# Kernel tuning notes

Measured on AMD Instinct MI355X. Metric: run time of the kernel, lower is better.

The kernel has to match this reference:

```python
import jax, jax.numpy as jnp
import numpy as np

N = 50000          # num nodes
E = 800000         # num edges
NUM_CLASSES = 40
FEAT_DIM = 256
FEAT_HID = 64
DEG_HID = 32
HID = 128
IN_CH = NUM_CLASSES + FEAT_HID + DEG_HID  # 136
MAX_DEG = 256      # degree-embedding table size (clip; random graph max deg << 256)


def _init_linear(key, fan_in, fan_out):
    kw, kb = jax.random.split(key)
    s = 1.0 / np.sqrt(fan_in)
    W = jax.random.uniform(kw, (fan_in, fan_out), jnp.float32, -s, s)
    b = jax.random.uniform(kb, (fan_out,), jnp.float32, -s, s)
    return W, b


def setup_inputs() -> dict:
    key = jax.random.key(0)
    ks = jax.random.split(key, 8)
    logits = jax.random.normal(ks[0], (N, NUM_CLASSES), jnp.float32)
    features = jax.random.normal(ks[1], (N, FEAT_DIM), jnp.float32)
    edge_index = jax.random.randint(ks[2], (2, E), 0, N, jnp.int32)
    Wf, bf = _init_linear(ks[3], FEAT_DIM, FEAT_HID)
    deg_table = jax.random.normal(ks[4], (MAX_DEG, DEG_HID), jnp.float32)
    W1, b1 = _init_linear(ks[5], IN_CH, HID)
    W2, b2 = _init_linear(ks[6], HID, HID)
    W3, b3 = _init_linear(ks[7], HID, NUM_CLASSES)
    return {"logits": logits, "features": features, "edge_index": edge_index,
            "Wf": Wf, "bf": bf, "deg_table": deg_table,
            "W1": W1, "b1": b1, "W2": W2, "b2": b2, "W3": W3, "b3": b3}


def reference(logits, features, edge_index, Wf, bf, deg_table, W1, b1, W2, b2, W3, b3):
    src, dst = edge_index[0], edge_index[1]
    # degree embedding: deg = degree(src) + degree(dst) on original edges
    ones_e = jnp.ones(src.shape[0], logits.dtype)
    deg = jax.ops.segment_sum(ones_e, src, num_segments=N) + \
          jax.ops.segment_sum(ones_e, dst, num_segments=N)
    deg_idx = jnp.clip(deg.astype(jnp.int32), 0, MAX_DEG - 1)
    deg_emb = deg_table[deg_idx]                              # [N, DEG_HID]

    x = jnp.concatenate([logits, features @ Wf + bf, deg_emb], axis=-1)  # [N, 136]

    # GCN normalization with self-loops (PyG gcn_norm): deg from dst column
    loop = jnp.arange(N, dtype=src.dtype)
    s = jnp.concatenate([src, loop])
    d = jnp.concatenate([dst, loop])
    dg = jax.ops.segment_sum(jnp.ones(d.shape[0], x.dtype), d, num_segments=N)
    dinv = jnp.where(dg > 0, jax.lax.rsqrt(dg), 0.0)
    norm = dinv[s] * dinv[d]                                  # [E+N]

    def conv(h, W, b):
        h = h @ W                                             # linear first
        msg = h[s] * norm[:, None]                            # gather + scale
        return jax.ops.segment_sum(msg, d, num_segments=N) + b

    x = jax.nn.relu(conv(x, W1, b1))   # dropout identity (inference)
    x = jax.nn.relu(conv(x, W2, b2))
    return conv(x, W3, b3)             # [N, NUM_CLASSES]
```

## Files before the change

kernel.cpp:

```cpp
#include <hip/hip_runtime.h>
#include <hip/hip_bf16.h>

constexpr int cN = 50000;
constexpr int cE = 800000;
constexpr int cNUM_CLASSES = 40;
constexpr int cFEAT_DIM = 256;
constexpr int cFEAT_HID = 64;
constexpr int cDEG_HID = 32;
constexpr int cHID = 128;
constexpr int cMAX_DEG = 256;
constexpr int cKF = 352;
constexpr int cLSTR = 40;

constexpr int cNCHUNK = 128;
constexpr int cCHUNK  = cE / cNCHUNK;
constexpr int cWORDS  = cN / 2;
constexpr int cHWORDS = cWORDS / 2;
constexpr int cSCANB  = (cWORDS + 255) / 256;

typedef unsigned short ushort8_t __attribute__((ext_vector_type(8)));
typedef short short8_t __attribute__((ext_vector_type(8)));
typedef float float4_t __attribute__((ext_vector_type(4)));

__device__ __forceinline__ unsigned short f2bf(float f) {
    unsigned u = __builtin_bit_cast(unsigned, f);
    u += 0x7fff + ((u >> 16) & 1);
    return (unsigned short)(u >> 16);
}
__device__ __forceinline__ float bf2f(unsigned short s) {
    unsigned u = ((unsigned)s) << 16;
    return __builtin_bit_cast(float, u);
}

__global__ __launch_bounds__(256) void prep_kernel(const int* __restrict__ edge,
                                                   unsigned* __restrict__ partial,
                                                   const float* __restrict__ Wf,
                                                   const float* __restrict__ bfv,
                                                   const float* __restrict__ W1,
                                                   const float* __restrict__ W2,
                                                   const float* __restrict__ W3,
                                                   unsigned short* __restrict__ Btc,
                                                   unsigned short* __restrict__ Wt2,
                                                   unsigned short* __restrict__ Wt3,
                                                   float* __restrict__ bias2,
                                                   int* __restrict__ desc) {
    __shared__ unsigned lds[cHWORDS];
    const int b = blockIdx.x, tid = threadIdx.x;
    if (b < 512) {
        const int cb = b & (cNCHUNK - 1);
        const int half = (b >> 7) & 1;
        const int which = b >> 8;
        for (int i = tid; i < cHWORDS; i += 256) lds[i] = 0;
        __syncthreads();
        const int* ids = edge + (size_t)which * cE + (size_t)cb * cCHUNK;
        const int lo = half * (cN / 2), hi = lo + cN / 2;
        const int wbase = half * cHWORDS;
        for (int i = tid; i < cCHUNK; i += 256) {
            int v = ids[i];
            if (v >= lo && v < hi)
                atomicAdd(&lds[(v >> 1) - wbase], 1u << ((v & 1) * 16));
        }
        __syncthreads();
        unsigned* outp = partial + ((size_t)which * cNCHUNK + cb) * cWORDS + wbase;
        for (int i = tid; i < cHWORDS; i += 256) outp[i] = lds[i];
        return;
    }
    if (b < 648) {
        int i = (b - 512) * 256 + tid;
        if (i < 12288) {
            int n = i / 96, r = i - (i / 96) * 96;
            unsigned short v;
            if (r < 40)       v = f2bf(W1[r * cHID + n]);
            else if (r < 72)  v = f2bf(W1[(104 + r - 40) * cHID + n]);
            else              v = 0;
            int k = (r < 40) ? r : (r < 72 ? 296 + (r - 40) : 328 + (r - 72));
            Btc[n * cKF + k] = v;
            return;
        }
        i -= 12288;
        if (i < 16384) {
            int n = i >> 7, k = i & 127;
            Wt2[n * cHID + k] = f2bf(W2[k * cHID + n]);
            return;
        }
        i -= 16384;
        if (i < 6144) {
            int n = i >> 7, k = i & 127;
            Wt3[n * cHID + k] = (n < cNUM_CLASSES) ? f2bf(W3[k * cNUM_CLASSES + n]) : 0;
        }
        return;
    }
    if (b < 776) {
        int i = (b - 648) * 256 + tid;
        int kf = i >> 7, n = i & 127;
        float s = 0.f;
        #pragma unroll 8
        for (int j = 0; j < cFEAT_HID; ++j)
            s += Wf[kf * cFEAT_HID + j] * W1[(40 + j) * cHID + n];
        Btc[n * cKF + 40 + kf] = f2bf(s);
        return;
    }
    if (tid < cHID) {
        float s = 0.f;
        #pragma unroll 8
        for (int j = 0; j < cFEAT_HID; ++j)
            s += bfv[j] * W1[(40 + j) * cHID + tid];
        bias2[tid] = s;
    } else if (tid - 128 < cSCANB) {
        desc[tid - 128] = 0;
    }
}

__global__ __launch_bounds__(256) void mega_scan_kernel(unsigned* __restrict__ partial,
                                                        int* __restrict__ rowptr,
                                                        float* __restrict__ dinv,
                                                        int* __restrict__ degidx,
                                                        int* __restrict__ desc) {
    const int b = blockIdx.x, tid = threadIdx.x;
    const int w = b * 256 + tid;
    unsigned slo = 0, shi = 0, plo = 0, phi = 0;
    if (w < cWORDS) {
        const unsigned* ps = partial + w;
        for (int c = 0; c < cNCHUNK; ++c) {
            unsigned v = ps[(size_t)c * cWORDS];
            slo += v & 0xFFFFu; shi += v >> 16;
        }
        unsigned* pd = partial + (size_t)cNCHUNK * cWORDS + w;
        for (int c = 0; c < cNCHUNK; ++c) {
            unsigned v = pd[(size_t)c * cWORDS];
            pd[(size_t)c * cWORDS] = plo | (phi << 16);
            plo += v & 0xFFFFu; phi += v >> 16;
        }
        int d0 = (int)(slo + plo), d1 = (int)(shi + phi);
        degidx[2 * w]     = d0 > cMAX_DEG - 1 ? cMAX_DEG - 1 : d0;
        degidx[2 * w + 1] = d1 > cMAX_DEG - 1 ? cMAX_DEG - 1 : d1;
    }
    __shared__ int s[256];
    int tot = (int)(plo + phi);
    s[tid] = tot;
    __syncthreads();
    #pragma unroll
    for (int off = 1; off < 256; off <<= 1) {
        int t = (tid >= off) ? s[tid - off] : 0;
        __syncthreads();
        s[tid] += t;
        __syncthreads();
    }
    int ex_local = s[tid] - tot;
    int block_total = s[255];
    if (tid == 0) atomicExch(&desc[b], block_total + 1);
    if (tid < b) {
        int v;
        do { v = atomicAdd(&desc[tid], 0); } while (v == 0);
        s[tid] = v - 1;
    }
    __syncthreads();
    if (tid >= b) s[tid] = 0;
    __syncthreads();
    #pragma unroll
    for (int off = 128; off > 0; off >>= 1) {
        if (tid < off) s[tid] += s[tid + off];
        __syncthreads();
    }
    int base = s[0] + ex_local;
    if (w < cWORDS) {
        rowptr[2 * w]     = base;
        rowptr[2 * w + 1] = base + (int)plo;
        dinv[2 * w]     = rsqrtf((float)(plo + 1));
        dinv[2 * w + 1] = rsqrtf((float)(phi + 1));
    }
    if (b == 0 && tid == 0) rowptr[cN] = cE;
}

__global__ __launch_bounds__(256) void scatter2_kernel(const int* __restrict__ edge,
                                                       const unsigned* __restrict__ partial,
                                                       const int* __restrict__ rowptr,
                                                       int* __restrict__ adj) {
    __shared__ unsigned lds[cHWORDS];
    const int b = blockIdx.x, tid = threadIdx.x;
    const int cb = b & (cNCHUNK - 1);
    const int half = b >> 7;
    const int wbase = half * cHWORDS;
    const unsigned* pp = partial + ((size_t)cNCHUNK + cb) * cWORDS + wbase;
    for (int i = tid; i < cHWORDS; i += 256) lds[i] = pp[i];
    __syncthreads();
    const int* srcs = edge + (size_t)cb * cCHUNK;
    const int* dsts = edge + cE + (size_t)cb * cCHUNK;
    const int lo = half * (cN / 2), hi = lo + cN / 2;
    for (int i = tid; i < cCHUNK; i += 256) {
        int d = dsts[i];
        if (d >= lo && d < hi) {
            int sh = (d & 1) * 16;
            unsigned old = atomicAdd(&lds[(d >> 1) - wbase], 1u << sh);
            int off = (int)((old >> sh) & 0xFFFFu);
            adj[rowptr[d] + off] = srcs[i];
        }
    }
}

__global__ __launch_bounds__(256) void gemm_fused(const float* __restrict__ logits,
                                                  const float* __restrict__ features,
                                                  const float* __restrict__ deg_table,
                                                  const int* __restrict__ degidx,
                                                  const unsigned short* __restrict__ Btc,
                                                  const float* __restrict__ bias2,
                                                  unsigned short* __restrict__ out) {
    constexpr int NT = 8;
    __shared__ unsigned short As[64 * cLSTR];
    __shared__ unsigned short Bs[NT * 16 * cLSTR];

    const int tid = threadIdx.x;
    const int wave = tid >> 6;
    const int lane = tid & 63;
    const int m15 = lane & 15;
    const int q = lane >> 4;
    const int rowbase = blockIdx.x * 64;

    float4_t acc[NT];
    #pragma unroll
    for (int t = 0; t < NT; ++t) acc[t] = (float4_t){0.f, 0.f, 0.f, 0.f};

    const int arow = tid >> 2;
    const int akq = (tid & 3) * 8;
    int gr = rowbase + arow;
    if (gr > cN - 1) gr = cN - 1;
    const int didx = degidx[gr];

    for (int k0 = 0; k0 < cKF; k0 += 32) {
        float4 v[2];
        #pragma unroll
        for (int h = 0; h < 2; ++h) {
            int k4 = k0 + akq + h * 4;
            v[h] = make_float4(0.f, 0.f, 0.f, 0.f);
            if (k4 < 40)       v[h] = *(const float4*)&logits[(size_t)gr * cNUM_CLASSES + k4];
            else if (k4 < 296) v[h] = *(const float4*)&features[(size_t)gr * cFEAT_DIM + (k4 - 40)];
            else if (k4 < 328) v[h] = *(const float4*)&deg_table[didx * cDEG_HID + (k4 - 296)];
        }
        ushort8_t o = { f2bf(v[0].x), f2bf(v[0].y), f2bf(v[0].z), f2bf(v[0].w),
                        f2bf(v[1].x), f2bf(v[1].y), f2bf(v[1].z), f2bf(v[1].w) };
        *(ushort8_t*)&As[arow * cLSTR + akq] = o;
        for (int i = tid; i < NT * 64; i += 256) {
            int n = i >> 2;
            int kq = (i & 3) * 8;
            *(ushort8_t*)&Bs[n * cLSTR + kq] = *(const ushort8_t*)&Btc[(size_t)n * cKF + k0 + kq];
        }
        __syncthreads();

        short8_t a = *(const short8_t*)&As[(wave * 16 + m15) * cLSTR + q * 8];
        #pragma unroll
        for (int t = 0; t < NT; ++t) {
            short8_t bfr = *(const short8_t*)&Bs[(t * 16 + m15) * cLSTR + q * 8];
            acc[t] = __builtin_amdgcn_mfma_f32_16x16x32_bf16(a, bfr, acc[t], 0, 0, 0);
        }
        __syncthreads();
    }

    #pragma unroll
    for (int t = 0; t < NT; ++t) {
        int col = t * 16 + m15;
        float bv = bias2[col];
        #pragma unroll
        for (int r = 0; r < 4; ++r) {
            int row = rowbase + wave * 16 + q * 4 + r;
            if (row < cN)
                out[(size_t)row * cHID + col] = f2bf(acc[t][r] + bv);
        }
    }
}

template <int KTOT, int NT, int OSTR, int OUTC>
__global__ __launch_bounds__(256) void mfma_gemm(const unsigned short* __restrict__ A,
                                                 const unsigned short* __restrict__ Bt,
                                                 unsigned short* __restrict__ out) {
    __shared__ unsigned short As[64 * cLSTR];
    __shared__ unsigned short Bs[NT * 16 * cLSTR];

    const int tid = threadIdx.x;
    const int wave = tid >> 6;
    const int lane = tid & 63;
    const int m15 = lane & 15;
    const int q = lane >> 4;
    const int rowbase = blockIdx.x * 64;

    float4_t acc[NT];
    #pragma unroll
    for (int t = 0; t < NT; ++t) acc[t] = (float4_t){0.f, 0.f, 0.f, 0.f};

    const int arow = tid >> 2;
    const int akq = (tid & 3) * 8;
    int gr = rowbase + arow;
    if (gr > cN - 1) gr = cN - 1;

    for (int k0 = 0; k0 < KTOT; k0 += 32) {
        *(ushort8_t*)&As[arow * cLSTR + akq] =
            *(const ushort8_t*)&A[(size_t)gr * KTOT + k0 + akq];
        for (int i = tid; i < NT * 64; i += 256) {
            int n = i >> 2;
            int kq = (i & 3) * 8;
            *(ushort8_t*)&Bs[n * cLSTR + kq] = *(const ushort8_t*)&Bt[(size_t)n * KTOT + k0 + kq];
        }
        __syncthreads();

        short8_t a = *(const short8_t*)&As[(wave * 16 + m15) * cLSTR + q * 8];
        #pragma unroll
        for (int t = 0; t < NT; ++t) {
            short8_t b = *(const short8_t*)&Bs[(t * 16 + m15) * cLSTR + q * 8];
            acc[t] = __builtin_amdgcn_mfma_f32_16x16x32_bf16(a, b, acc[t], 0, 0, 0);
        }
        __syncthreads();
    }

    #pragma unroll
    for (int t = 0; t < NT; ++t) {
        int col = t * 16 + m15;
        if (OUTC % 16 != 0 && col >= OUTC) continue;
        #pragma unroll
        for (int r = 0; r < 4; ++r) {
            int row = rowbase + wave * 16 + q * 4 + r;
            if (row < cN)
                out[(size_t)row * OSTR + col] = f2bf(acc[t][r]);
        }
    }
}

template <bool RELU>
__global__ __launch_bounds__(128) void agg_bf128(const unsigned short* __restrict__ t,
                                                 const int* __restrict__ rowptr,
                                                 const int* __restrict__ adj,
                                                 const float* __restrict__ dinv,
                                                 const float* __restrict__ b,
                                                 unsigned short* __restrict__ outb) {
    const int tid = threadIdx.x;
    const int lane = tid & 15;
    const int row = blockIdx.x * 8 + (tid >> 4);
    if (row >= cN) return;
    const int c = lane * 8;
    const float di = dinv[row];
    int e = rowptr[row];
    const int end = rowptr[row + 1];
    float a0[8], a1[8];
    #pragma unroll
    for (int k = 0; k < 8; ++k) { a0[k] = 0.f; a1[k] = 0.f; }
    for (; e + 1 < end; e += 2) {
        int j0 = adj[e], j1 = adj[e + 1];
        float v0 = dinv[j0], v1 = dinv[j1];
        ushort8_t t0 = *(const ushort8_t*)&t[(size_t)j0 * cHID + c];
        ushort8_t t1 = *(const ushort8_t*)&t[(size_t)j1 * cHID + c];
        #pragma unroll
        for (int k = 0; k < 8; ++k) {
            a0[k] += v0 * bf2f(t0[k]);
            a1[k] += v1 * bf2f(t1[k]);
        }
    }
    if (e < end) {
        int j0 = adj[e];
        float v0 = dinv[j0];
        ushort8_t t0 = *(const ushort8_t*)&t[(size_t)j0 * cHID + c];
        #pragma unroll
        for (int k = 0; k < 8; ++k) a0[k] += v0 * bf2f(t0[k]);
    }
    ushort8_t ts = *(const ushort8_t*)&t[(size_t)row * cHID + c];
    const float d2 = di * di;
    ushort8_t o;
    #pragma unroll
    for (int k = 0; k < 8; ++k) {
        float r = di * (a0[k] + a1[k]) + d2 * bf2f(ts[k]) + b[c + k];
        if (RELU) r = fmaxf(r, 0.f);
        o[k] = f2bf(r);
    }
    *(ushort8_t*)&outb[(size_t)row * cHID + c] = o;
}

__global__ __launch_bounds__(128) void agg_bf40(const unsigned short* __restrict__ t,
                                                const int* __restrict__ rowptr,
                                                const int* __restrict__ adj,
                                                const float* __restrict__ dinv,
                                                const float* __restrict__ b,
                                                float* __restrict__ out) {
    const int tid = threadIdx.x;
    const int lane = tid & 7;
    const int row = blockIdx.x * 16 + (tid >> 3);
    if (row >= cN) return;
    const int c = lane * 8;
    if (c >= cNUM_CLASSES) return;
    const float di = dinv[row];
    int e = rowptr[row];
    const int end = rowptr[row + 1];
    float a0[8], a1[8];
    #pragma unroll
    for (int k = 0; k < 8; ++k) { a0[k] = 0.f; a1[k] = 0.f; }
    for (; e + 1 < end; e += 2) {
        int j0 = adj[e], j1 = adj[e + 1];
        float v0 = dinv[j0], v1 = dinv[j1];
        ushort8_t t0 = *(const ushort8_t*)&t[(size_t)j0 * cNUM_CLASSES + c];
        ushort8_t t1 = *(const ushort8_t*)&t[(size_t)j1 * cNUM_CLASSES + c];
        #pragma unroll
        for (int k = 0; k < 8; ++k) {
            a0[k] += v0 * bf2f(t0[k]);
            a1[k] += v1 * bf2f(t1[k]);
        }
    }
    if (e < end) {
        int j0 = adj[e];
        float v0 = dinv[j0];
        ushort8_t t0 = *(const ushort8_t*)&t[(size_t)j0 * cNUM_CLASSES + c];
        #pragma unroll
        for (int k = 0; k < 8; ++k) a0[k] += v0 * bf2f(t0[k]);
    }
    ushort8_t ts = *(const ushort8_t*)&t[(size_t)row * cNUM_CLASSES + c];
    const float d2 = di * di;
    float r[8];
    #pragma unroll
    for (int k = 0; k < 8; ++k) r[k] = di * (a0[k] + a1[k]) + d2 * bf2f(ts[k]) + b[c + k];
    float4 v0 = make_float4(r[0], r[1], r[2], r[3]);
    float4 v1 = make_float4(r[4], r[5], r[6], r[7]);
    *(float4*)&out[(size_t)row * cNUM_CLASSES + c] = v0;
    *(float4*)&out[(size_t)row * cNUM_CLASSES + c + 4] = v1;
}

extern "C" void kernel_launch(void* const* d_in, const int* in_sizes, int n_in,
                              void* d_out, int out_size, void* d_ws, size_t ws_size,
                              hipStream_t stream) {
    const float* logits    = (const float*)d_in[0];
    const float* features  = (const float*)d_in[1];
    const int*   edge      = (const int*)d_in[2];
    const float* Wf        = (const float*)d_in[3];
    const float* bfv       = (const float*)d_in[4];
    const float* deg_table = (const float*)d_in[5];
    const float* W1        = (const float*)d_in[6];
    const float* b1        = (const float*)d_in[7];
    const float* W2        = (const float*)d_in[8];
    const float* b2        = (const float*)d_in[9];
    const float* W3        = (const float*)d_in[10];
    const float* b3        = (const float*)d_in[11];
    float* out = (float*)d_out;

    int* rowptr    = (int*)d_ws;
    int* adj       = rowptr + cN + 16;
    int* desc      = adj + cE;
    int* degidx    = desc + 128;
    float* dinv    = (float*)(degidx + cN);
    float* bias2   = dinv + cN;
    unsigned short* tb  = (unsigned short*)(bias2 + 128);
    unsigned short* hb  = tb + (size_t)cN * cHID;
    unsigned short* Btc = hb + (size_t)cN * cHID;
    unsigned short* Wt2 = Btc + 128 * cKF;
    unsigned short* Wt3 = Wt2 + 128 * cHID;
    unsigned* partial = (unsigned*)(Wt3 + 48 * cHID);

    prep_kernel<<<777, 256, 0, stream>>>(edge, partial, Wf, bfv, W1, W2, W3,
                                         Btc, Wt2, Wt3, bias2, desc);

    mega_scan_kernel<<<cSCANB, 256, 0, stream>>>(partial, rowptr, dinv, degidx, desc);

    scatter2_kernel<<<256, 256, 0, stream>>>(edge, partial, rowptr, adj);

    constexpr int MB = (cN + 63) / 64;

    gemm_fused<<<MB, 256, 0, stream>>>(logits, features, deg_table, degidx, Btc, bias2, tb);
    agg_bf128<true><<<(cN + 7) / 8, 128, 0, stream>>>(tb, rowptr, adj, dinv, b1, hb);

    mfma_gemm<cHID, 8, cHID, cHID><<<MB, 256, 0, stream>>>(hb, Wt2, tb);
    agg_bf128<true><<<(cN + 7) / 8, 128, 0, stream>>>(tb, rowptr, adj, dinv, b2, hb);

    mfma_gemm<cHID, 3, cNUM_CLASSES, cNUM_CLASSES><<<MB, 256, 0, stream>>>(hb, Wt3, tb);
    agg_bf40<<<(cN + 15) / 16, 128, 0, stream>>>(tb, rowptr, adj, dinv, b3, out);
}
```

Baseline: 297.2 us.

## Load MFMA operands directly from global memory, dropping LDS staging and barriers

Both the fused input GEMM and the generic MFMA GEMM no longer stage A and B tiles through shared memory. Each lane now loads its own A fragment row and B fragment straight from global memory into registers, and the k-loop is fully unrolled with no __syncthreads. This removes LDS traffic and barrier stalls. In exchange, each wave re-reads the B matrix from global memory and cache instead of sharing it, and register pressure rises from the unrolled loads.

```diff
diff --git a/kernel.cpp b/kernel.cpp
--- a/kernel.cpp
+++ b/kernel.cpp
@@ -10,7 +10,6 @@
 constexpr int cHID = 128;
 constexpr int cMAX_DEG = 256;
 constexpr int cKF = 352;
-constexpr int cLSTR = 40;
 
 constexpr int cNCHUNK = 128;
 constexpr int cCHUNK  = cE / cNCHUNK;
@@ -206,9 +205,6 @@
                                                   const float* __restrict__ bias2,
                                                   unsigned short* __restrict__ out) {
     constexpr int NT = 8;
-    __shared__ unsigned short As[64 * cLSTR];
-    __shared__ unsigned short Bs[NT * 16 * cLSTR];
-
     const int tid = threadIdx.x;
     const int wave = tid >> 6;
     const int lane = tid & 63;
@@ -216,43 +212,35 @@
     const int q = lane >> 4;
     const int rowbase = blockIdx.x * 64;
 
-    float4_t acc[NT];
-    #pragma unroll
-    for (int t = 0; t < NT; ++t) acc[t] = (float4_t){0.f, 0.f, 0.f, 0.f};
-
-    const int arow = tid >> 2;
-    const int akq = (tid & 3) * 8;
-    int gr = rowbase + arow;
+    int gr = rowbase + wave * 16 + m15;
     if (gr > cN - 1) gr = cN - 1;
     const int didx = degidx[gr];
 
+    float4_t acc[NT];
+    #pragma unroll
+    for (int t = 0; t < NT; ++t) acc[t] = (float4_t){0.f, 0.f, 0.f, 0.f};
+
+    const float* lrow = logits + (size_t)gr * cNUM_CLASSES;
+    const float* frow = features + (size_t)gr * cFEAT_DIM;
+    const float* drow = deg_table + (size_t)didx * cDEG_HID;
+    const unsigned short* brow = Btc + m15 * cKF + q * 8;
+
+    #pragma unroll
     for (int k0 = 0; k0 < cKF; k0 += 32) {
-        float4 v[2];
-        #pragma unroll
-        for (int h = 0; h < 2; ++h) {
-            int k4 = k0 + akq + h * 4;
-            v[h] = make_float4(0.f, 0.f, 0.f, 0.f);
-            if (k4 < 40)       v[h] = *(const float4*)&logits[(size_t)gr * cNUM_CLASSES + k4];
-            else if (k4 < 296) v[h] = *(const float4*)&features[(size_t)gr * cFEAT_DIM + (k4 - 40)];
-            else if (k4 < 328) v[h] = *(const float4*)&deg_table[didx * cDEG_HID + (k4 - 296)];
-        }
-        ushort8_t o = { f2bf(v[0].x), f2bf(v[0].y), f2bf(v[0].z), f2bf(v[0].w),
-                        f2bf(v[1].x), f2bf(v[1].y), f2bf(v[1].z), f2bf(v[1].w) };
-        *(ushort8_t*)&As[arow * cLSTR + akq] = o;
-        for (int i = tid; i < NT * 64; i += 256) {
-            int n = i >> 2;
-            int kq = (i & 3) * 8;
-            *(ushort8_t*)&Bs[n * cLSTR + kq] = *(const ushort8_t*)&Btc[(size_t)n * cKF + k0 + kq];
-        }
-        __syncthreads();
-
-        short8_t a = *(const short8_t*)&As[(wave * 16 + m15) * cLSTR + q * 8];
+        const int k4 = k0 + q * 8;
+        float4 v0 = make_float4(0.f, 0.f, 0.f, 0.f);
+        float4 v1 = make_float4(0.f, 0.f, 0.f, 0.f);
+        if (k4 < 40)       { v0 = *(const float4*)&lrow[k4];       v1 = *(const float4*)&lrow[k4 + 4]; }
+        else if (k4 < 296) { v0 = *(const float4*)&frow[k4 - 40];  v1 = *(const float4*)&frow[k4 - 36]; }
+        else if (k4 < 328) { v0 = *(const float4*)&drow[k4 - 296]; v1 = *(const float4*)&drow[k4 - 292]; }
+        short8_t a;
+        a[0] = (short)f2bf(v0.x); a[1] = (short)f2bf(v0.y); a[2] = (short)f2bf(v0.z); a[3] = (short)f2bf(v0.w);
+        a[4] = (short)f2bf(v1.x); a[5] = (short)f2bf(v1.y); a[6] = (short)f2bf(v1.z); a[7] = (short)f2bf(v1.w);
         #pragma unroll
         for (int t = 0; t < NT; ++t) {
-            short8_t bfr = *(const short8_t*)&Bs[(t * 16 + m15) * cLSTR + q * 8];
-            acc[t] = __builtin_amdgcn_mfma_f32_16x16x32_bf16(a, bfr, acc[t], 0, 0, 0);
-        }
-        __syncthreads();
+            short8_t bb = *(const short8_t*)&brow[(size_t)t * 16 * cKF + k0];
+            acc[t] = __builtin_amdgcn_mfma_f32_16x16x32_bf16(a, bb, acc[t], 0, 0, 0);
+        }
     }
 
     #pragma unroll
@@ -272,9 +260,6 @@
 __global__ __launch_bounds__(256) void mfma_gemm(const unsigned short* __restrict__ A,
                                                  const unsigned short* __restrict__ Bt,
                                                  unsigned short* __restrict__ out) {
-    __shared__ unsigned short As[64 * cLSTR];
-    __shared__ unsigned short Bs[NT * 16 * cLSTR];
-
     const int tid = threadIdx.x;
     const int wave = tid >> 6;
     const int lane = tid & 63;
@@ -282,32 +267,24 @@
     const int q = lane >> 4;
     const int rowbase = blockIdx.x * 64;
 
+    int gr = rowbase + wave * 16 + m15;
+    if (gr > cN - 1) gr = cN - 1;
+
     float4_t acc[NT];
     #pragma unroll
     for (int t = 0; t < NT; ++t) acc[t] = (float4_t){0.f, 0.f, 0.f, 0.f};
 
-    const int arow = tid >> 2;
-    const int akq = (tid & 3) * 8;
-    int gr = rowbase + arow;
-    if (gr > cN - 1) gr = cN - 1;
-
+    const unsigned short* arow = A + (size_t)gr * KTOT + q * 8;
+    const unsigned short* brow = Bt + m15 * KTOT + q * 8;
+
+    #pragma unroll
     for (int k0 = 0; k0 < KTOT; k0 += 32) {
-        *(ushort8_t*)&As[arow * cLSTR + akq] =
-            *(const ushort8_t*)&A[(size_t)gr * KTOT + k0 + akq];
-        for (int i = tid; i < NT * 64; i += 256) {
-            int n = i >> 2;
-            int kq = (i & 3) * 8;
-            *(ushort8_t*)&Bs[n * cLSTR + kq] = *(const ushort8_t*)&Bt[(size_t)n * KTOT + k0 + kq];
-        }
-        __syncthreads();
-
-        short8_t a = *(const short8_t*)&As[(wave * 16 + m15) * cLSTR + q * 8];
+        short8_t a = *(const short8_t*)&arow[k0];
         #pragma unroll
         for (int t = 0; t < NT; ++t) {
-            short8_t b = *(const short8_t*)&Bs[(t * 16 + m15) * cLSTR + q * 8];
+            short8_t b = *(const short8_t*)&brow[(size_t)t * 16 * KTOT + k0];
             acc[t] = __builtin_amdgcn_mfma_f32_16x16x32_bf16(a, b, acc[t], 0, 0, 0);
         }
-        __syncthreads();
     }
 
     #pragma unroll
```

Result: slower. 322.8 us (+8.6%).
